# Performance work log

Measured on AMD Instinct MI355X. Metric: run time of the kernel, lower is better.

## Reference

```python
import jax, jax.numpy as jnp
import numpy as np

N = 100_000        # nodes
E = 1_600_000      # edges (avg degree 16)
D = 64             # in_feats == hidden_dim
L = 5              # 2 conv-wo-resnet + 3 resnet layers
G = 64             # graphs in the batch
RES_START = 2      # residual connections start at layer index 2
EPS = 1e-5
SLOPE = 0.01       # leaky_relu default negative slope


def setup_inputs() -> dict:
    key = jax.random.key(0)
    ks = jax.random.split(key, 9)
    s = 1.0 / np.sqrt(D)
    return {
        "x": jax.random.normal(ks[0], (N, D), jnp.float32),
        "edge_index": jax.random.randint(ks[1], (2, E), 0, N, dtype=jnp.int32),
        "batch": jnp.sort(jax.random.randint(ks[2], (N,), 0, G, dtype=jnp.int32)),
        "W_l": (jax.random.normal(ks[3], (L, D, D), jnp.float32) * s),   # neighbor lin
        "W_r": (jax.random.normal(ks[4], (L, D, D), jnp.float32) * s),   # root lin
        "b":   (jax.random.normal(ks[5], (L, D), jnp.float32) * s),
        "gn_w":  jnp.ones((L, D), jnp.float32) + 0.1 * jax.random.normal(ks[6], (L, D), jnp.float32),
        "gn_b":  0.1 * jax.random.normal(ks[7], (L, D), jnp.float32),
        "gn_ms": jnp.ones((L, D), jnp.float32) + 0.1 * jax.random.normal(ks[8], (L, D), jnp.float32),
    }


def _mean_agg(x, src, dst):
    # mean aggregation of x[src] into dst (SAGEConv 'mean' aggr)
    summed = jax.ops.segment_sum(x[src], dst, num_segments=N)           # [N, D]
    deg = jax.ops.segment_sum(jnp.ones((src.shape[0],), x.dtype), dst, num_segments=N)
    return summed / jnp.maximum(deg, 1.0)[:, None]


def _sage_bidir(x, edge_index, Wl, Wr, b):
    src, dst = edge_index[0], edge_index[1]
    root = x @ Wr + b
    out_f = _mean_agg(x, src, dst) @ Wl + root
    out_b = _mean_agg(x, dst, src) @ Wl + root   # flipped edges
    return 0.5 * (out_f + out_b)


def _graph_norm(x, batch, w, bias, mean_scale):
    cnt = jnp.maximum(jax.ops.segment_sum(jnp.ones((N,), x.dtype), batch, num_segments=G), 1.0)
    mean = jax.ops.segment_sum(x, batch, num_segments=G) / cnt[:, None]    # [G, D]
    out = x - mean_scale * mean[batch]
    var = jax.ops.segment_sum(out * out, batch, num_segments=G) / cnt[:, None]
    out = out * jax.lax.rsqrt(var + EPS)[batch]
    return w * out + bias


def reference(x, edge_index, batch, W_l, W_r, b, gn_w, gn_b, gn_ms):
    h = x
    for i in range(L):
        h_new = _sage_bidir(h, edge_index, W_l[i], W_r[i], b[i])
        h_new = _graph_norm(h_new, batch, gn_w[i], gn_b[i], gn_ms[i])
        h_new = jnp.where(h_new >= 0, h_new, SLOPE * h_new)   # leaky_relu
        # dropout is identity in eval mode
        h = h_new if i < RES_START else h + h_new
    cnt = jnp.maximum(jax.ops.segment_sum(jnp.ones((N,), h.dtype), batch, num_segments=G), 1.0)
    return jax.ops.segment_sum(h, batch, num_segments=G) / cnt[:, None]   # global_mean_pool [G, D]
```

## Files before the change

### kernel.cpp

```cpp
#include <hip/hip_runtime.h>

#define DD 64
#define GG 64
#define EPSV 1e-5f
#define SLOPE 0.01f

#define NRM_NPW 16
#define NV_WN 32

#define NRANGE 512
#define RSHIFT 8
#define NPR 256
#define ABLK 512

typedef unsigned short ushort_t;
typedef unsigned int uint_t;
typedef float v2f __attribute__((ext_vector_type(2)));
typedef __attribute__((ext_vector_type(8))) short bf16x8;
typedef __attribute__((ext_vector_type(4))) float f32x4;

__device__ __forceinline__ ushort_t f2bf(float f) {
  uint_t u = __float_as_uint(f);
  uint_t r = (u + 0x7fffu + ((u >> 16) & 1u)) >> 16;
  return (ushort_t)r;
}
__device__ __forceinline__ float bf2f(ushort_t s) { return __uint_as_float(((uint_t)s) << 16); }
__device__ __forceinline__ v2f unpk(uint_t u) {
  v2f r;
  r.x = __uint_as_float(u << 16);
  r.y = __uint_as_float(u & 0xffff0000u);
  return r;
}

__global__ __launch_bounds__(256) void bin_count_kernel(const int* __restrict__ src,
                                                        const int* __restrict__ dst,
                                                        int* __restrict__ hist, int E) {
  __shared__ int cf[NRANGE], cb[NRANGE];
  for (int i=threadIdx.x; i<NRANGE; i+=256) { cf[i]=0; cb[i]=0; }
  __syncthreads();
  int epb = (E + ABLK-1)/ABLK;
  int lo = blockIdx.x*epb, hi = lo+epb; if (hi>E) hi=E;
  for (int e=lo+threadIdx.x; e<hi; e+=256) {
    int d = __builtin_nontemporal_load(&dst[e]);
    int s = __builtin_nontemporal_load(&src[e]);
    atomicAdd(&cf[d>>RSHIFT], 1);
    atomicAdd(&cb[s>>RSHIFT], 1);
  }
  __syncthreads();
  for (int r=threadIdx.x; r<NRANGE; r+=256) {
    hist[(size_t)r*ABLK + blockIdx.x]            = cf[r];
    hist[(size_t)(NRANGE+r)*ABLK + blockIdx.x]   = cb[r];
  }
}

__global__ void block_sum_kernel(const int* __restrict__ v, int* __restrict__ partial, int M) {
  __shared__ int sm[1024];
  int i = blockIdx.x*1024 + threadIdx.x;
  sm[threadIdx.x] = (i<M) ? v[i] : 0;
  __syncthreads();
  for (int s=512; s>0; s>>=1) {
    if (threadIdx.x < s) sm[threadIdx.x] += sm[threadIdx.x+s];
    __syncthreads();
  }
  if (threadIdx.x==0) partial[blockIdx.x] = sm[0];
}

__global__ void scan_partial_kernel(int* __restrict__ partial, int nb) {
  __shared__ int sm[512];
  int t = threadIdx.x;
  int v = (t<nb) ? partial[t] : 0;
  int orig = v;
  sm[t] = v; __syncthreads();
  for (int off=1; off<512; off<<=1) {
    int a = (t>=off) ? sm[t-off] : 0;
    __syncthreads();
    v += a; sm[t] = v;
    __syncthreads();
  }
  if (t<nb) partial[t] = v - orig;
}

__global__ void scan_apply_kernel(const int* __restrict__ v, const int* __restrict__ partial,
                                  int* __restrict__ out, int M) {
  __shared__ int sm[1024];
  int i = blockIdx.x*1024 + threadIdx.x;
  int x = (i<M) ? v[i] : 0;
  int orig = x;
  sm[threadIdx.x] = x; __syncthreads();
  for (int off=1; off<1024; off<<=1) {
    int a = (threadIdx.x>=off) ? sm[threadIdx.x-off] : 0;
    __syncthreads();
    x += a; sm[threadIdx.x] = x;
    __syncthreads();
  }
  if (i<M) out[i] = x - orig + partial[blockIdx.x];
}

__global__ __launch_bounds__(256) void bin_scatter_kernel(const int* __restrict__ src,
                                                          const int* __restrict__ dst,
                                                          const int* __restrict__ offs,
                                                          int* __restrict__ staged, int E) {
  __shared__ int ofF[NRANGE], ofB[NRANGE];
  for (int r=threadIdx.x; r<NRANGE; r+=256) {
    ofF[r] = offs[(size_t)r*ABLK + blockIdx.x];
    ofB[r] = offs[(size_t)(NRANGE+r)*ABLK + blockIdx.x];
  }
  __syncthreads();
  int epb = (E + ABLK-1)/ABLK;
  int lo = blockIdx.x*epb, hi = lo+epb; if (hi>E) hi=E;
  for (int e=lo+threadIdx.x; e<hi; e+=256) {
    int d = __builtin_nontemporal_load(&dst[e]);
    int s = __builtin_nontemporal_load(&src[e]);
    int pf = atomicAdd(&ofF[d>>RSHIFT], 1);
    staged[pf] = (s << 8) | (d & (NPR-1));
    int pb = atomicAdd(&ofB[s>>RSHIFT], 1);
    staged[pb] = (d << 8) | (s & (NPR-1));
  }
}

__global__ __launch_bounds__(256) void range_fill_kernel(const int* __restrict__ staged,
                                                         const int* __restrict__ offs,
                                                         int* __restrict__ rp_f, int* __restrict__ rp_b,
                                                         int* __restrict__ col_f, int* __restrict__ col_b,
                                                         int N, int E) {
  __shared__ int cnt[NPR], noff[NPR], sc[NPR];
  int lr = blockIdx.x;
  int d = lr >> 9, r = lr & (NRANGE-1);
  int start = offs[(size_t)lr*ABLK];
  int end   = (lr+1 < 2*NRANGE) ? offs[(size_t)(lr+1)*ABLK] : 2*E;
  int t = threadIdx.x;
  cnt[t] = 0; __syncthreads();
  for (int k=start+t; k<end; k+=256) {
    atomicAdd(&cnt[staged[k] & (NPR-1)], 1);
  }
  __syncthreads();
  int x = cnt[t]; sc[t] = x; __syncthreads();
  for (int off=1; off<NPR; off<<=1) {
    int a = (t>=off) ? sc[t-off] : 0;
    __syncthreads();
    x += a; sc[t] = x;
    __syncthreads();
  }
  noff[t] = x - cnt[t];
  __syncthreads();
  int base = d ? (start - E) : start;
  int node = (r << RSHIFT) + t;
  int* rp = d ? rp_b : rp_f;
  if (node < N)       rp[node] = base + noff[t];
  else if (node == N) rp[N]    = base + noff[t];
  cnt[t] = 0; __syncthreads();
  int* col = d ? col_b : col_f;
  for (int k=start+t; k<end; k+=256) {
    int rec = staged[k];
    int li = rec & (NPR-1);
    int rank = atomicAdd(&cnt[li], 1);
    col[base + noff[li] + rank] = rec >> 8;
  }
}

__global__ void cnt_kernel(const int* __restrict__ batch, int* __restrict__ cnt, int N) {
  __shared__ int hist[GG];
  if (threadIdx.x < GG) hist[threadIdx.x] = 0;
  __syncthreads();
  int i = blockIdx.x*blockDim.x + threadIdx.x;
  int stride = gridDim.x*blockDim.x;
  for (int n=i; n<N; n+=stride) atomicAdd(&hist[batch[n]], 1);
  __syncthreads();
  if (threadIdx.x < GG) atomicAdd(&cnt[threadIdx.x], hist[threadIdx.x]);
}

__global__ void tobf16_kernel(const float* __restrict__ in, ushort_t* __restrict__ out, int M) {
  int i = blockIdx.x*blockDim.x + threadIdx.x;
  int stride = gridDim.x*blockDim.x;
  for (int k=i; k<M; k+=stride) out[k] = f2bf(in[k]);
}

__global__ void wpack_kernel(const float* __restrict__ Wl, const float* __restrict__ Wr,
                             ushort_t* __restrict__ Wb) {
  int l = blockIdx.x;
  const float* wl = Wl + (size_t)l*4096;
  const float* wr = Wr + (size_t)l*4096;
  ushort_t* out = Wb + (size_t)l*8192;
  for (int idx = threadIdx.x; idx < 8192; idx += 256) {
    int kb = idx >> 9, rem = idx & 511, col = rem >> 3, j = rem & 7;
    int k = kb*8 + j;
    float v = (k < 64) ? wl[(size_t)k*64+col] : wr[(size_t)(k-64)*64+col];
    out[idx] = f2bf(v);
  }
}

__global__ __launch_bounds__(256) void gather_kernel(
    const ushort_t* __restrict__ hb,
    const int* __restrict__ rp_f, const int* __restrict__ col_f,
    const int* __restrict__ rp_b, const int* __restrict__ col_b,
    ushort_t* __restrict__ sbufb, int N)
{
  int w = (blockIdx.x*(blockDim.x>>6)) + (threadIdx.x>>6);
  if (w >= N) return;
  int lane = threadIdx.x & 63;
  int qt = lane >> 4;
  int g  = lane & 15;
  const char* hbb = (const char*)hb;
  uint_t goff = (uint_t)g << 3;

  v2f a01={0.f,0.f}, a23={0.f,0.f}, c01={0.f,0.f}, c23={0.f,0.f};
  int degf, degb;

  {
    int s0 = rp_f[w], e0 = rp_f[w+1];
    degf = e0 - s0;
    for (int base=s0; base<e0; base+=64) {
      int m = e0-base; if (m>64) m=64;
      int jv = (lane<m) ? col_f[base+lane] : 0;
      int q=0;
      for (; 4*q+16 <= m; q+=4) {
        int j0=__shfl(jv,4*q+qt),    j1=__shfl(jv,4*q+4+qt);
        int j2=__shfl(jv,4*q+8+qt),  j3=__shfl(jv,4*q+12+qt);
        uint2 v0 = *(const uint2*)(hbb + ((((uint_t)j0)<<7) | goff));
        uint2 v1 = *(const uint2*)(hbb + ((((uint_t)j1)<<7) | goff));
        uint2 v2 = *(const uint2*)(hbb + ((((uint_t)j2)<<7) | goff));
        uint2 v3 = *(const uint2*)(hbb + ((((uint_t)j3)<<7) | goff));
        a01 += unpk(v0.x); a23 += unpk(v0.y);
        a01 += unpk(v1.x); a23 += unpk(v1.y);
        a01 += unpk(v2.x); a23 += unpk(v2.y);
        a01 += unpk(v3.x); a23 += unpk(v3.y);
      }
      for (; 4*q+qt < m; ++q) {
        int j=__shfl(jv,4*q+qt);
        uint2 v = *(const uint2*)(hbb + ((((uint_t)j)<<7) | goff));
        a01 += unpk(v.x); a23 += unpk(v.y);
      }
    }
  }
  {
    int s1 = rp_b[w], e1 = rp_b[w+1];
    degb = e1 - s1;
    for (int base=s1; base<e1; base+=64) {
      int m = e1-base; if (m>64) m=64;
      int jv = (lane<m) ? col_b[base+lane] : 0;
      int q=0;
      for (; 4*q+16 <= m; q+=4) {
        int j0=__shfl(jv,4*q+qt),    j1=__shfl(jv,4*q+4+qt);
        int j2=__shfl(jv,4*q+8+qt),  j3=__shfl(jv,4*q+12+qt);
        uint2 v0 = *(const uint2*)(hbb + ((((uint_t)j0)<<7) | goff));
        uint2 v1 = *(const uint2*)(hbb + ((((uint_t)j1)<<7) | goff));
        uint2 v2 = *(const uint2*)(hbb + ((((uint_t)j2)<<7) | goff));
        uint2 v3 = *(const uint2*)(hbb + ((((uint_t)j3)<<7) | goff));
        c01 += unpk(v0.x); c23 += unpk(v0.y);
        c01 += unpk(v1.x); c23 += unpk(v1.y);
        c01 += unpk(v2.x); c23 += unpk(v2.y);
        c01 += unpk(v3.x); c23 += unpk(v3.y);
      }
      for (; 4*q+qt < m; ++q) {
        int j=__shfl(jv,4*q+qt);
        uint2 v = *(const uint2*)(hbb + ((((uint_t)j)<<7) | goff));
        c01 += unpk(v.x); c23 += unpk(v.y);
      }
    }
  }

  float df = fmaxf((float)degf, 1.f);
  float db = fmaxf((float)degb, 1.f);
  float s0v = 0.5f*(a01.x/df + c01.x/db);
  float s1v = 0.5f*(a01.y/df + c01.y/db);
  float s2v = 0.5f*(a23.x/df + c23.x/db);
  float s3v = 0.5f*(a23.y/df + c23.y/db);
  s0v += __shfl_xor(s0v,16); s0v += __shfl_xor(s0v,32);
  s1v += __shfl_xor(s1v,16); s1v += __shfl_xor(s1v,32);
  s2v += __shfl_xor(s2v,16); s2v += __shfl_xor(s2v,32);
  s3v += __shfl_xor(s3v,16); s3v += __shfl_xor(s3v,32);
  if (qt==0) {
    uint_t p0 = (uint_t)f2bf(s0v) | ((uint_t)f2bf(s1v) << 16);
    uint_t p1 = (uint_t)f2bf(s2v) | ((uint_t)f2bf(s3v) << 16);
    *(uint2*)&((uint_t*)sbufb)[(size_t)w*32 + 2*g] = make_uint2(p0, p1);
  }
}

__global__ __launch_bounds__(256) void gemm_kernel(
    const ushort_t* __restrict__ hb, const ushort_t* __restrict__ sbufb,
    const ushort_t* __restrict__ Wb, const float* __restrict__ bias,
    const int* __restrict__ batch,
    ushort_t* __restrict__ tb, float* __restrict__ gsum, float* __restrict__ gsq, int N)
{
  __shared__ float lsum[8][DD];
  __shared__ float lsq[8][DD];
  __shared__ ushort_t tbs[64][DD];

  int wid = threadIdx.x >> 6;
  int lane = threadIdx.x & 63;
  int lrow = lane & 15;
  int lk   = lane >> 4;
  int base = blockIdx.x*64;
  int strip = base + wid*16;

  int g0 = batch[(base < N) ? base : (N-1)];
  for (int i=threadIdx.x; i<8*DD; i+=256) { (&lsum[0][0])[i]=0.f; (&lsq[0][0])[i]=0.f; }

  int arow = strip + lrow; if (arow >= N) arow = N-1;
  const bf16x8* sfrag = (const bf16x8*)(sbufb + (size_t)arow*DD);
  const bf16x8* hfrag = (const bf16x8*)(hb    + (size_t)arow*DD);
  bf16x8 a0 = sfrag[lk];
  bf16x8 a1 = sfrag[4+lk];
  bf16x8 a2 = hfrag[lk];
  bf16x8 a3 = hfrag[4+lk];

  const bf16x8* wbp = (const bf16x8*)Wb;
  f32x4 acc[4];
  #pragma unroll
  for (int t=0; t<4; ++t) acc[t] = (f32x4){0.f,0.f,0.f,0.f};

  #pragma unroll
  for (int t=0; t<4; ++t) {
    int col = t*16 + lrow;
    bf16x8 b0 = wbp[(0*4+lk)*64 + col];
    bf16x8 b1 = wbp[(1*4+lk)*64 + col];
    bf16x8 b2 = wbp[(2*4+lk)*64 + col];
    bf16x8 b3 = wbp[(3*4+lk)*64 + col];
    acc[t] = __builtin_amdgcn_mfma_f32_16x16x32_bf16(a0, b0, acc[t], 0,0,0);
    acc[t] = __builtin_amdgcn_mfma_f32_16x16x32_bf16(a1, b1, acc[t], 0,0,0);
    acc[t] = __builtin_amdgcn_mfma_f32_16x16x32_bf16(a2, b2, acc[t], 0,0,0);
    acc[t] = __builtin_amdgcn_mfma_f32_16x16x32_bf16(a3, b3, acc[t], 0,0,0);
  }
  __syncthreads();

  int bt[4];
  #pragma unroll
  for (int r=0; r<4; ++r) {
    int node = strip + lk*4 + r;
    bt[r] = (node < N) ? batch[node] : -1;
  }
  #pragma unroll
  for (int t=0; t<4; ++t) {
    int feat = t*16 + lrow;
    float bv = bias[feat];
    int gcur = -1; float ga=0.f, qa=0.f;
    #pragma unroll
    for (int r=0; r<4; ++r) {
      if (bt[r] < 0) break;
      int node = strip + lk*4 + r;
      float v = acc[t][r] + bv;
      tbs[node-base][feat] = f2bf(v);
      if (bt[r] != gcur) {
        if (gcur >= 0) {
          int slot = gcur - g0;
          if (slot < 8) { atomicAdd(&lsum[slot][feat], ga); atomicAdd(&lsq[slot][feat], qa); }
          else { atomicAdd(&gsum[gcur*DD+feat], ga); atomicAdd(&gsq[gcur*DD+feat], qa); }
        }
        gcur = bt[r]; ga = 0.f; qa = 0.f;
      }
      ga += v; qa += v*v;
    }
    if (gcur >= 0) {
      int slot = gcur - g0;
      if (slot < 8) { atomicAdd(&lsum[slot][feat], ga); atomicAdd(&lsq[slot][feat], qa); }
      else { atomicAdd(&gsum[gcur*DD+feat], ga); atomicAdd(&gsq[gcur*DD+feat], qa); }
    }
  }
  __syncthreads();

  int lastnode = base+63; if (lastnode >= N) lastnode = N-1;
  int nslots = batch[lastnode] - g0 + 1; if (nslots > 8) nslots = 8;
  for (int idx=threadIdx.x; idx < nslots*DD; idx += 256) {
    int s = idx >> 6, f = idx & 63;
    float vs = lsum[s][f], vq = lsq[s][f];
    if (vs != 0.f || vq != 0.f) {
      atomicAdd(&gsum[(g0+s)*DD+f], vs);
      atomicAdd(&gsq[(g0+s)*DD+f], vq);
    }
  }
  for (int c=threadIdx.x; c<512; c+=256) {
    int row = c >> 3, off = (c & 7)*8;
    int node = base + row;
    if (node < N) *(bf16x8*)&tb[(size_t)node*DD + off] = *(const bf16x8*)&tbs[row][off];
  }
}

__global__ __launch_bounds__(256) void norm2v_kernel(
    const ushort_t* __restrict__ tb,
    const float* __restrict__ gsum, const float* __restrict__ gsq,
    const int* __restrict__ cnt, const int* __restrict__ batch,
    const float* __restrict__ gw, const float* __restrict__ gb,
    const float* __restrict__ gms,
    ushort_t* __restrict__ hb, int resid, int N)
{
  int wv_id = (blockIdx.x*blockDim.x + threadIdx.x) >> 6;
  int lane = threadIdx.x & 63;
  int oct = lane & 7;
  int no  = lane >> 3;
  int base = wv_id * NV_WN;
  if (base >= N) return;
  float wvv[8], bvv[8], msv[8];
  #pragma unroll
  for (int j=0;j<8;++j){ int f=oct*8+j; wvv[j]=gw[f]; bvv[j]=gb[f]; msv[j]=gms[f]; }
  int gcur=-1; float mean[8], rs[8];
  int end = base + NV_WN; if (end > N) end = N;
  for (int nb=base+no; nb<end; nb+=8) {
    int g = batch[nb];
    if (g != gcur) {
      float invc = 1.f/fmaxf((float)cnt[g],1.f);
      #pragma unroll
      for (int j=0;j<8;++j){
        int f = oct*8+j;
        float mn = gsum[g*DD+f]*invc;
        float mq = gsq[g*DD+f]*invc;
        float var = mq - msv[j]*(2.f-msv[j])*mn*mn;
        mean[j]=mn; rs[j]=rsqrtf(var+EPSV);
      }
      gcur=g;
    }
    bf16x8 tv = *(const bf16x8*)&tb[(size_t)nb*DD + oct*8];
    bf16x8 hv8 = *(const bf16x8*)&hb[(size_t)nb*DD + oct*8];
    bf16x8 outv;
    #pragma unroll
    for (int j=0;j<8;++j){
      float u = bf2f((ushort_t)tv[j]) - msv[j]*mean[j];
      float y = wvv[j]*u*rs[j] + bvv[j];
      y = (y>=0.f) ? y : SLOPE*y;
      float hvv = resid ? (bf2f((ushort_t)hv8[j]) + y) : y;
      outv[j] = (short)f2bf(hvv);
    }
    *(bf16x8*)&hb[(size_t)nb*DD + oct*8] = outv;
  }
}

__global__ void norm2_last_kernel(const ushort_t* __restrict__ tb,
                             const float* __restrict__ gsum, const float* __restrict__ gsq,
                             const int* __restrict__ cnt, const int* __restrict__ batch,
                             const float* __restrict__ gw, const float* __restrict__ gb,
                             const float* __restrict__ gms,
                             const ushort_t* __restrict__ hb,
                             float* __restrict__ pout, int N)
{
  int wid = (blockIdx.x*blockDim.x + threadIdx.x) >> 6;
  int lane = threadIdx.x & 63;
  int base = wid*NRM_NPW;
  if (base >= N) return;
  float wv = gw[lane], bv = gb[lane], msv = gms[lane];
  float cms = msv*(2.f - msv);
  int gcur=-1; float rs=0.f, mean=0.f, pacc=0.f;
  int end = base+NRM_NPW; if (end>N) end=N;
  for (int node=base; node<end; ++node) {
    int g = batch[node];
    if (g!=gcur) {
      if (gcur>=0) atomicAdd(&pout[gcur*DD+lane], pacc);
      pacc = 0.f;
      float invc = 1.f/fmaxf((float)cnt[g],1.f);
      mean = gsum[g*DD+lane]*invc;
      float msq = gsq[g*DD+lane]*invc;
      float var = msq - cms*mean*mean;
      rs = rsqrtf(var + EPSV);
      gcur=g;
    }
    float u = bf2f(tb[(size_t)node*DD+lane]) - msv*mean;
    float y = wv*u*rs + bv;
    y = (y>=0.f) ? y : SLOPE*y;
    pacc += bf2f(hb[(size_t)node*DD+lane]) + y;
  }
  if (gcur>=0) atomicAdd(&pout[gcur*DD+lane], pacc);
}

__global__ void finalize_kernel(const float* __restrict__ pout, const int* __restrict__ cnt,
                                float* __restrict__ out)
{
  int i = blockIdx.x*blockDim.x + threadIdx.x;
  if (i < GG*DD) {
    float invc = 1.f/fmaxf((float)cnt[i>>6],1.f);
    out[i] = pout[i]*invc;
  }
}

extern "C" void kernel_launch(void* const* d_in, const int* in_sizes, int n_in,
                              void* d_out, int out_size, void* d_ws, size_t ws_size,
                              hipStream_t stream)
{
  const float* x    = (const float*)d_in[0];
  const int*  ei    = (const int*)d_in[1];
  const int*  batch = (const int*)d_in[2];
  const float* W_l  = (const float*)d_in[3];
  const float* W_r  = (const float*)d_in[4];
  const float* bias = (const float*)d_in[5];
  const float* gn_w = (const float*)d_in[6];
  const float* gn_b = (const float*)d_in[7];
  const float* gn_ms= (const float*)d_in[8];

  int N = in_sizes[2];
  int E = in_sizes[1]/2;
  int L = in_sizes[5]/DD;
  const int* src = ei;
  const int* dst = ei + E;

  char* p = (char*)d_ws;
  int*   cnt   = (int*)p;   p += GG*4;
  float* gsum  = (float*)p; p += (size_t)L*GG*DD*4;
  float* gsq   = (float*)p; p += (size_t)L*GG*DD*4;
  float* pout  = (float*)p; p += GG*DD*4;
  size_t zeroBytes = (char*)p - (char*)d_ws;

  int* staged  = (int*)p; p += (size_t)2*E*4;
  ushort_t* tb    = (ushort_t*)p; p += (size_t)N*DD*2;
  ushort_t* sbufb = (ushort_t*)p; p += (size_t)N*DD*2;
  ushort_t* hb    = (ushort_t*)p; p += (size_t)N*DD*2;
  ushort_t* wb    = (ushort_t*)p; p += (size_t)L*8192*2;
  int* rp_f    = (int*)p; p += (size_t)(N+1)*4;
  int* rp_b    = (int*)p; p += (size_t)(N+1)*4;
  int* col_f   = (int*)p; p += (size_t)E*4;
  int* col_b   = (int*)p; p += (size_t)E*4;
  int* hist    = (int*)p; p += (size_t)2*NRANGE*ABLK*4;
  int* offs    = (int*)p; p += (size_t)2*NRANGE*ABLK*4;
  int* partial = (int*)p; p += 512*4;

  hipMemsetAsync(d_ws, 0, zeroBytes, stream);

  const int M = 2*NRANGE*ABLK;
  bin_count_kernel<<<ABLK, 256, 0, stream>>>(src, dst, hist, E);
  block_sum_kernel<<<(M+1023)/1024, 1024, 0, stream>>>(hist, partial, M);
  scan_partial_kernel<<<1, 512, 0, stream>>>(partial, (M+1023)/1024);
  scan_apply_kernel<<<(M+1023)/1024, 1024, 0, stream>>>(hist, partial, offs, M);
  bin_scatter_kernel<<<ABLK, 256, 0, stream>>>(src, dst, offs, staged, E);
  range_fill_kernel<<<2*NRANGE, 256, 0, stream>>>(staged, offs, rp_f, rp_b, col_f, col_b, N, E);

  cnt_kernel<<<391, 256, 0, stream>>>(batch, cnt, N);
  tobf16_kernel<<<2048, 256, 0, stream>>>(x, hb, N*DD);
  wpack_kernel<<<L, 256, 0, stream>>>(W_l, W_r, wb);

  int gthBlocks = (N + 3)/4;
  int agBlocks = (N + 63)/64;
  int nvWaves = (N + NV_WN-1)/NV_WN;
  int nvBlocks = (nvWaves+3)/4;
  int nrmWaves = (N + NRM_NPW-1)/NRM_NPW;
  int nrmBlocks = (nrmWaves+3)/4;

  for (int i=0; i<L; ++i) {
    float* gsum_i = gsum + (size_t)i*GG*DD;
    float* gsq_i  = gsq  + (size_t)i*GG*DD;
    gather_kernel<<<gthBlocks, 256, 0, stream>>>(hb, rp_f, col_f, rp_b, col_b, sbufb, N);
    gemm_kernel<<<agBlocks, 256, 0, stream>>>(hb, sbufb, wb + (size_t)i*8192,
                                              bias+(size_t)i*DD, batch, tb, gsum_i, gsq_i, N);
    if (i < L-1) {
      norm2v_kernel<<<nvBlocks, 256, 0, stream>>>(tb, gsum_i, gsq_i, cnt, batch,
                                                  gn_w+(size_t)i*DD, gn_b+(size_t)i*DD,
                                                  gn_ms+(size_t)i*DD, hb, (i>=2)?1:0, N);
    } else {
      norm2_last_kernel<<<nrmBlocks, 256, 0, stream>>>(tb, gsum_i, gsq_i, cnt, batch,
                                                       gn_w+(size_t)i*DD, gn_b+(size_t)i*DD,
                                                       gn_ms+(size_t)i*DD, hb, pout, N);
    }
  }
  finalize_kernel<<<16, 256, 0, stream>>>(pout, cnt, (float*)d_out);
}
```

Baseline: 671.1 us.

## Fuse neighbor gather and MFMA GEMM into one kernel via shared-memory rows

Merges the gather kernel and the GEMM/stat kernel into a single kernel. Each 256-thread block gathers 16 nodes, with each wave handling 4 nodes, and stages the aggregated bf16 rows in LDS. Each wave then computes one 16-column tile of the output with MFMA. This removes the sbufb global round trip and one launch per layer. In exchange, blocks are smaller (16 nodes), the GEMM tile is shared across waves, and there are more per-block stat atomics and barriers. Waves that drew low-degree nodes can also sit idle waiting on the barrier.

```diff
diff --git a/kernel.cpp b/kernel.cpp
--- a/kernel.cpp
+++ b/kernel.cpp
@@ -189,161 +189,148 @@
   }
 }
 
-__global__ __launch_bounds__(256) void gather_kernel(
+__global__ __launch_bounds__(256) void gg_kernel(
     const ushort_t* __restrict__ hb,
     const int* __restrict__ rp_f, const int* __restrict__ col_f,
     const int* __restrict__ rp_b, const int* __restrict__ col_b,
-    ushort_t* __restrict__ sbufb, int N)
-{
-  int w = (blockIdx.x*(blockDim.x>>6)) + (threadIdx.x>>6);
-  if (w >= N) return;
-  int lane = threadIdx.x & 63;
-  int qt = lane >> 4;
-  int g  = lane & 15;
-  const char* hbb = (const char*)hb;
-  uint_t goff = (uint_t)g << 3;
-
-  v2f a01={0.f,0.f}, a23={0.f,0.f}, c01={0.f,0.f}, c23={0.f,0.f};
-  int degf, degb;
-
-  {
-    int s0 = rp_f[w], e0 = rp_f[w+1];
-    degf = e0 - s0;
-    for (int base=s0; base<e0; base+=64) {
-      int m = e0-base; if (m>64) m=64;
-      int jv = (lane<m) ? col_f[base+lane] : 0;
-      int q=0;
-      for (; 4*q+16 <= m; q+=4) {
-        int j0=__shfl(jv,4*q+qt),    j1=__shfl(jv,4*q+4+qt);
-        int j2=__shfl(jv,4*q+8+qt),  j3=__shfl(jv,4*q+12+qt);
-        uint2 v0 = *(const uint2*)(hbb + ((((uint_t)j0)<<7) | goff));
-        uint2 v1 = *(const uint2*)(hbb + ((((uint_t)j1)<<7) | goff));
-        uint2 v2 = *(const uint2*)(hbb + ((((uint_t)j2)<<7) | goff));
-        uint2 v3 = *(const uint2*)(hbb + ((((uint_t)j3)<<7) | goff));
-        a01 += unpk(v0.x); a23 += unpk(v0.y);
-        a01 += unpk(v1.x); a23 += unpk(v1.y);
-        a01 += unpk(v2.x); a23 += unpk(v2.y);
-        a01 += unpk(v3.x); a23 += unpk(v3.y);
-      }
-      for (; 4*q+qt < m; ++q) {
-        int j=__shfl(jv,4*q+qt);
-        uint2 v = *(const uint2*)(hbb + ((((uint_t)j)<<7) | goff));
-        a01 += unpk(v.x); a23 += unpk(v.y);
-      }
-    }
-  }
-  {
-    int s1 = rp_b[w], e1 = rp_b[w+1];
-    degb = e1 - s1;
-    for (int base=s1; base<e1; base+=64) {
-      int m = e1-base; if (m>64) m=64;
-      int jv = (lane<m) ? col_b[base+lane] : 0;
-      int q=0;
-      for (; 4*q+16 <= m; q+=4) {
-        int j0=__shfl(jv,4*q+qt),    j1=__shfl(jv,4*q+4+qt);
-        int j2=__shfl(jv,4*q+8+qt),  j3=__shfl(jv,4*q+12+qt);
-        uint2 v0 = *(const uint2*)(hbb + ((((uint_t)j0)<<7) | goff));
-        uint2 v1 = *(const uint2*)(hbb + ((((uint_t)j1)<<7) | goff));
-        uint2 v2 = *(const uint2*)(hbb + ((((uint_t)j2)<<7) | goff));
-        uint2 v3 = *(const uint2*)(hbb + ((((uint_t)j3)<<7) | goff));
-        c01 += unpk(v0.x); c23 += unpk(v0.y);
-        c01 += unpk(v1.x); c23 += unpk(v1.y);
-        c01 += unpk(v2.x); c23 += unpk(v2.y);
-        c01 += unpk(v3.x); c23 += unpk(v3.y);
-      }
-      for (; 4*q+qt < m; ++q) {
-        int j=__shfl(jv,4*q+qt);
-        uint2 v = *(const uint2*)(hbb + ((((uint_t)j)<<7) | goff));
-        c01 += unpk(v.x); c23 += unpk(v.y);
-      }
-    }
-  }
-
-  float df = fmaxf((float)degf, 1.f);
-  float db = fmaxf((float)degb, 1.f);
-  float s0v = 0.5f*(a01.x/df + c01.x/db);
-  float s1v = 0.5f*(a01.y/df + c01.y/db);
-  float s2v = 0.5f*(a23.x/df + c23.x/db);
-  float s3v = 0.5f*(a23.y/df + c23.y/db);
-  s0v += __shfl_xor(s0v,16); s0v += __shfl_xor(s0v,32);
-  s1v += __shfl_xor(s1v,16); s1v += __shfl_xor(s1v,32);
-  s2v += __shfl_xor(s2v,16); s2v += __shfl_xor(s2v,32);
-  s3v += __shfl_xor(s3v,16); s3v += __shfl_xor(s3v,32);
-  if (qt==0) {
-    uint_t p0 = (uint_t)f2bf(s0v) | ((uint_t)f2bf(s1v) << 16);
-    uint_t p1 = (uint_t)f2bf(s2v) | ((uint_t)f2bf(s3v) << 16);
-    *(uint2*)&((uint_t*)sbufb)[(size_t)w*32 + 2*g] = make_uint2(p0, p1);
-  }
-}
-
-__global__ __launch_bounds__(256) void gemm_kernel(
-    const ushort_t* __restrict__ hb, const ushort_t* __restrict__ sbufb,
     const ushort_t* __restrict__ Wb, const float* __restrict__ bias,
     const int* __restrict__ batch,
     ushort_t* __restrict__ tb, float* __restrict__ gsum, float* __restrict__ gsq, int N)
 {
-  __shared__ float lsum[8][DD];
-  __shared__ float lsq[8][DD];
-  __shared__ ushort_t tbs[64][DD];
+  __shared__ ushort_t srow[16][72];
+  __shared__ float lsum[4][DD];
+  __shared__ float lsq[4][DD];
+  __shared__ ushort_t tbs[16][DD];
 
   int wid = threadIdx.x >> 6;
   int lane = threadIdx.x & 63;
+  int base = blockIdx.x*16;
+
+  for (int i=threadIdx.x; i<4*DD; i+=256) { (&lsum[0][0])[i]=0.f; (&lsq[0][0])[i]=0.f; }
+
+  {
+    int qt = lane >> 4;
+    int g  = lane & 15;
+    const char* hbb = (const char*)hb;
+    uint_t goff = (uint_t)g << 3;
+
+    for (int nn=0; nn<4; ++nn) {
+      int w = base + wid*4 + nn;
+      v2f a01={0.f,0.f}, a23={0.f,0.f}, c01={0.f,0.f}, c23={0.f,0.f};
+      int degf=0, degb=0;
+      if (w < N) {
+        {
+          int s0 = rp_f[w], e0 = rp_f[w+1];
+          degf = e0 - s0;
+          for (int bse=s0; bse<e0; bse+=64) {
+            int m = e0-bse; if (m>64) m=64;
+            int jv = (lane<m) ? col_f[bse+lane] : 0;
+            int q=0;
+            for (; 4*q+16 <= m; q+=4) {
+              int j0=__shfl(jv,4*q+qt),    j1=__shfl(jv,4*q+4+qt);
+              int j2=__shfl(jv,4*q+8+qt),  j3=__shfl(jv,4*q+12+qt);
+              uint2 v0 = *(const uint2*)(hbb + ((((uint_t)j0)<<7) | goff));
+              uint2 v1 = *(const uint2*)(hbb + ((((uint_t)j1)<<7) | goff));
+              uint2 v2 = *(const uint2*)(hbb + ((((uint_t)j2)<<7) | goff));
+              uint2 v3 = *(const uint2*)(hbb + ((((uint_t)j3)<<7) | goff));
+              a01 += unpk(v0.x); a23 += unpk(v0.y);
+              a01 += unpk(v1.x); a23 += unpk(v1.y);
+              a01 += unpk(v2.x); a23 += unpk(v2.y);
+              a01 += unpk(v3.x); a23 += unpk(v3.y);
+            }
+            for (; 4*q+qt < m; ++q) {
+              int j=__shfl(jv,4*q+qt);
+              uint2 v = *(const uint2*)(hbb + ((((uint_t)j)<<7) | goff));
+              a01 += unpk(v.x); a23 += unpk(v.y);
+            }
+          }
+        }
+        {
+          int s1 = rp_b[w], e1 = rp_b[w+1];
+          degb = e1 - s1;
+          for (int bse=s1; bse<e1; bse+=64) {
+            int m = e1-bse; if (m>64) m=64;
+            int jv = (lane<m) ? col_b[bse+lane] : 0;
+            int q=0;
+            for (; 4*q+16 <= m; q+=4) {
+              int j0=__shfl(jv,4*q+qt),    j1=__shfl(jv,4*q+4+qt);
+              int j2=__shfl(jv,4*q+8+qt),  j3=__shfl(jv,4*q+12+qt);
+              uint2 v0 = *(const uint2*)(hbb + ((((uint_t)j0)<<7) | goff));
+              uint2 v1 = *(const uint2*)(hbb + ((((uint_t)j1)<<7) | goff));
+              uint2 v2 = *(const uint2*)(hbb + ((((uint_t)j2)<<7) | goff));
+              uint2 v3 = *(const uint2*)(hbb + ((((uint_t)j3)<<7) | goff));
+              c01 += unpk(v0.x); c23 += unpk(v0.y);
+              c01 += unpk(v1.x); c23 += unpk(v1.y);
+              c01 += unpk(v2.x); c23 += unpk(v2.y);
+              c01 += unpk(v3.x); c23 += unpk(v3.y);
+            }
+            for (; 4*q+qt < m; ++q) {
+              int j=__shfl(jv,4*q+qt);
+              uint2 v = *(const uint2*)(hbb + ((((uint_t)j)<<7) | goff));
+              c01 += unpk(v.x); c23 += unpk(v.y);
+            }
+          }
+        }
+      }
+      float df = fmaxf((float)degf, 1.f);
+      float db = fmaxf((float)degb, 1.f);
+      float s0v = 0.5f*(a01.x/df + c01.x/db);
+      float s1v = 0.5f*(a01.y/df + c01.y/db);
+      float s2v = 0.5f*(a23.x/df + c23.x/db);
+      float s3v = 0.5f*(a23.y/df + c23.y/db);
+      s0v += __shfl_xor(s0v,16); s0v += __shfl_xor(s0v,32);
+      s1v += __shfl_xor(s1v,16); s1v += __shfl_xor(s1v,32);
+      s2v += __shfl_xor(s2v,16); s2v += __shfl_xor(s2v,32);
+      s3v += __shfl_xor(s3v,16); s3v += __shfl_xor(s3v,32);
+      if (qt==0) {
+        uint2 pk;
+        pk.x = (uint_t)f2bf(s0v) | ((uint_t)f2bf(s1v) << 16);
+        pk.y = (uint_t)f2bf(s2v) | ((uint_t)f2bf(s3v) << 16);
+        *(uint2*)&srow[wid*4+nn][4*g] = pk;
+      }
+    }
+  }
+  __syncthreads();
+
   int lrow = lane & 15;
   int lk   = lane >> 4;
-  int base = blockIdx.x*64;
-  int strip = base + wid*16;
-
-  int g0 = batch[(base < N) ? base : (N-1)];
-  for (int i=threadIdx.x; i<8*DD; i+=256) { (&lsum[0][0])[i]=0.f; (&lsq[0][0])[i]=0.f; }
-
-  int arow = strip + lrow; if (arow >= N) arow = N-1;
-  const bf16x8* sfrag = (const bf16x8*)(sbufb + (size_t)arow*DD);
-  const bf16x8* hfrag = (const bf16x8*)(hb    + (size_t)arow*DD);
-  bf16x8 a0 = sfrag[lk];
-  bf16x8 a1 = sfrag[4+lk];
+
+  const ushort_t* sr = &srow[lrow][0];
+  bf16x8 a0 = *(const bf16x8*)&sr[lk*8];
+  bf16x8 a1 = *(const bf16x8*)&sr[32+lk*8];
+  int arow = base + lrow; if (arow >= N) arow = N-1;
+  const bf16x8* hfrag = (const bf16x8*)(hb + (size_t)arow*DD);
   bf16x8 a2 = hfrag[lk];
   bf16x8 a3 = hfrag[4+lk];
 
   const bf16x8* wbp = (const bf16x8*)Wb;
-  f32x4 acc[4];
-  #pragma unroll
-  for (int t=0; t<4; ++t) acc[t] = (f32x4){0.f,0.f,0.f,0.f};
-
-  #pragma unroll
-  for (int t=0; t<4; ++t) {
-    int col = t*16 + lrow;
-    bf16x8 b0 = wbp[(0*4+lk)*64 + col];
-    bf16x8 b1 = wbp[(1*4+lk)*64 + col];
-    bf16x8 b2 = wbp[(2*4+lk)*64 + col];
-    bf16x8 b3 = wbp[(3*4+lk)*64 + col];
-    acc[t] = __builtin_amdgcn_mfma_f32_16x16x32_bf16(a0, b0, acc[t], 0,0,0);
-    acc[t] = __builtin_amdgcn_mfma_f32_16x16x32_bf16(a1, b1, acc[t], 0,0,0);
-    acc[t] = __builtin_amdgcn_mfma_f32_16x16x32_bf16(a2, b2, acc[t], 0,0,0);
-    acc[t] = __builtin_amdgcn_mfma_f32_16x16x32_bf16(a3, b3, acc[t], 0,0,0);
-  }
-  __syncthreads();
-
+  int col = wid*16 + lrow;
+  f32x4 acc = (f32x4){0.f,0.f,0.f,0.f};
+  acc = __builtin_amdgcn_mfma_f32_16x16x32_bf16(a0, wbp[(0*4+lk)*64 + col], acc, 0,0,0);
+  acc = __builtin_amdgcn_mfma_f32_16x16x32_bf16(a1, wbp[(1*4+lk)*64 + col], acc, 0,0,0);
+  acc = __builtin_amdgcn_mfma_f32_16x16x32_bf16(a2, wbp[(2*4+lk)*64 + col], acc, 0,0,0);
+  acc = __builtin_amdgcn_mfma_f32_16x16x32_bf16(a3, wbp[(3*4+lk)*64 + col], acc, 0,0,0);
+
+  int g0 = batch[(base < N) ? base : (N-1)];
   int bt[4];
   #pragma unroll
   for (int r=0; r<4; ++r) {
-    int node = strip + lk*4 + r;
+    int node = base + lk*4 + r;
     bt[r] = (node < N) ? batch[node] : -1;
   }
-  #pragma unroll
-  for (int t=0; t<4; ++t) {
-    int feat = t*16 + lrow;
+  {
+    int feat = wid*16 + lrow;
     float bv = bias[feat];
     int gcur = -1; float ga=0.f, qa=0.f;
     #pragma unroll
     for (int r=0; r<4; ++r) {
       if (bt[r] < 0) break;
-      int node = strip + lk*4 + r;
-      float v = acc[t][r] + bv;
-      tbs[node-base][feat] = f2bf(v);
+      float v = acc[r] + bv;
+      tbs[lk*4+r][feat] = f2bf(v);
       if (bt[r] != gcur) {
         if (gcur >= 0) {
           int slot = gcur - g0;
-          if (slot < 8) { atomicAdd(&lsum[slot][feat], ga); atomicAdd(&lsq[slot][feat], qa); }
+          if (slot < 4) { atomicAdd(&lsum[slot][feat], ga); atomicAdd(&lsq[slot][feat], qa); }
           else { atomicAdd(&gsum[gcur*DD+feat], ga); atomicAdd(&gsq[gcur*DD+feat], qa); }
         }
         gcur = bt[r]; ga = 0.f; qa = 0.f;
@@ -352,14 +339,14 @@
     }
     if (gcur >= 0) {
       int slot = gcur - g0;
-      if (slot < 8) { atomicAdd(&lsum[slot][feat], ga); atomicAdd(&lsq[slot][feat], qa); }
+      if (slot < 4) { atomicAdd(&lsum[slot][feat], ga); atomicAdd(&lsq[slot][feat], qa); }
       else { atomicAdd(&gsum[gcur*DD+feat], ga); atomicAdd(&gsq[gcur*DD+feat], qa); }
     }
   }
   __syncthreads();
 
-  int lastnode = base+63; if (lastnode >= N) lastnode = N-1;
-  int nslots = batch[lastnode] - g0 + 1; if (nslots > 8) nslots = 8;
+  int lastnode = base+15; if (lastnode >= N) lastnode = N-1;
+  int nslots = batch[lastnode] - g0 + 1; if (nslots > 4) nslots = 4;
   for (int idx=threadIdx.x; idx < nslots*DD; idx += 256) {
     int s = idx >> 6, f = idx & 63;
     float vs = lsum[s][f], vq = lsq[s][f];
@@ -368,7 +355,7 @@
       atomicAdd(&gsq[(g0+s)*DD+f], vq);
     }
   }
-  for (int c=threadIdx.x; c<512; c+=256) {
+  for (int c=threadIdx.x; c<128; c+=256) {
     int row = c >> 3, off = (c & 7)*8;
     int node = base + row;
     if (node < N) *(bf16x8*)&tb[(size_t)node*DD + off] = *(const bf16x8*)&tbs[row][off];
@@ -498,7 +485,6 @@
 
   int* staged  = (int*)p; p += (size_t)2*E*4;
   ushort_t* tb    = (ushort_t*)p; p += (size_t)N*DD*2;
-  ushort_t* sbufb = (ushort_t*)p; p += (size_t)N*DD*2;
   ushort_t* hb    = (ushort_t*)p; p += (size_t)N*DD*2;
   ushort_t* wb    = (ushort_t*)p; p += (size_t)L*8192*2;
   int* rp_f    = (int*)p; p += (size_t)(N+1)*4;
@@ -523,8 +509,7 @@
   tobf16_kernel<<<2048, 256, 0, stream>>>(x, hb, N*DD);
   wpack_kernel<<<L, 256, 0, stream>>>(W_l, W_r, wb);
 
-  int gthBlocks = (N + 3)/4;
-  int agBlocks = (N + 63)/64;
+  int ggBlocks = (N + 15)/16;
   int nvWaves = (N + NV_WN-1)/NV_WN;
   int nvBlocks = (nvWaves+3)/4;
   int nrmWaves = (N + NRM_NPW-1)/NRM_NPW;
@@ -533,9 +518,9 @@
   for (int i=0; i<L; ++i) {
     float* gsum_i = gsum + (size_t)i*GG*DD;
     float* gsq_i  = gsq  + (size_t)i*GG*DD;
-    gather_kernel<<<gthBlocks, 256, 0, stream>>>(hb, rp_f, col_f, rp_b, col_b, sbufb, N);
-    gemm_kernel<<<agBlocks, 256, 0, stream>>>(hb, sbufb, wb + (size_t)i*8192,
-                                              bias+(size_t)i*DD, batch, tb, gsum_i, gsq_i, N);
+    gg_kernel<<<ggBlocks, 256, 0, stream>>>(hb, rp_f, col_f, rp_b, col_b,
+                                            wb + (size_t)i*8192, bias+(size_t)i*DD,
+                                            batch, tb, gsum_i, gsq_i, N);
     if (i < L-1) {
       norm2v_kernel<<<nvBlocks, 256, 0, stream>>>(tb, gsum_i, gsq_i, cnt, batch,
                                                   gn_w+(size_t)i*DD, gn_b+(size_t)i*DD,
```

After: 647.8 us, median of 2. 1.04x faster.
